# Kernel tuning notes

Hardware: AMD Instinct MI355X
Metric: run time of the kernel (lower is better)

Reference implementation:

```python
import jax, jax.numpy as jnp
import numpy as np

N = 10000      # nodes
E = 160000     # edges
IN = 256       # input feature dim
HID = 128      # hidden per head
H = 4          # heads (all layers)
EMB = 128      # dim_embedding (last-layer out per head)
SLOPE = 0.2    # leaky_relu negative slope in attention


def _gat_layer(h, src, dst, W, al, ar, b, residual, apply_act):
    """DGL-style GATConv (no dropout). h: [N, F_in], W: [F_in, H*D], al/ar/b: [H, D]."""
    n = h.shape[0]
    heads, d = al.shape
    feat = (h @ W).reshape(n, heads, d)                 # [N, H, D]
    el = jnp.sum(feat * al, axis=-1)                    # [N, H]
    er = jnp.sum(feat * ar, axis=-1)                    # [N, H]
    e = jax.nn.leaky_relu(el[src] + er[dst], SLOPE)     # [E, H]
    # edge softmax over incoming edges of dst (numerically stable)
    m = jax.ops.segment_max(e, dst, num_segments=n)
    m = jnp.where(jnp.isfinite(m), m, 0.0)              # empty segments -> 0
    ex = jnp.exp(e - m[dst])
    den = jax.ops.segment_sum(ex, dst, num_segments=n)
    alpha = ex / jnp.maximum(den[dst], 1e-9)            # [E, H]
    rst = jax.ops.segment_sum(alpha[:, :, None] * feat[src], dst, num_segments=n)  # [N, H, D]
    if residual:
        rst = rst + h.reshape(n, heads, d)              # identity residual (dims match)
    rst = rst + b
    return jax.nn.elu(rst) if apply_act else rst


def setup_inputs() -> dict:
    key = jax.random.key(0)
    ks = jax.random.split(key, 24)
    def p(k, shape, scale):
        return (jax.random.normal(k, shape, jnp.float32) * scale)
    inp = {
        'x': jax.random.normal(ks[0], (N, IN), jnp.float32),
        'src': jax.random.randint(ks[1], (E,), 0, N, dtype=jnp.int32).astype(jnp.int64),
        'dst': jax.random.randint(ks[2], (E,), 0, N, dtype=jnp.int32).astype(jnp.int64),
        # layer 0: in=IN, out=HID per head
        'W0': p(ks[3], (IN, H * HID), 1.0 / np.sqrt(IN)),
        'al0': p(ks[4], (H, HID), 0.1), 'ar0': p(ks[5], (H, HID), 0.1),
        'b0': p(ks[6], (H, HID), 0.02),
        # layer 1: in=H*HID=512, out=HID per head, residual
        'W1': p(ks[7], (H * HID, H * HID), 1.0 / np.sqrt(H * HID)),
        'al1': p(ks[8], (H, HID), 0.1), 'ar1': p(ks[9], (H, HID), 0.1),
        'b1': p(ks[10], (H, HID), 0.02),
        # layer 2: in=H*HID=512, out=EMB per head, residual, no activation
        'W2': p(ks[11], (H * HID, H * EMB), 1.0 / np.sqrt(H * HID)),
        'al2': p(ks[12], (H, EMB), 0.1), 'ar2': p(ks[13], (H, EMB), 0.1),
        'b2': p(ks[14], (H, EMB), 0.02),
        # MLP predictor: 2*EMB -> EMB -> EMB//2 -> 1
        'Wm0': p(ks[15], (2 * EMB, EMB), 1.0 / np.sqrt(2 * EMB)), 'bm0': p(ks[16], (EMB,), 0.02),
        'Wm1': p(ks[17], (EMB, EMB // 2), 1.0 / np.sqrt(EMB)), 'bm1': p(ks[18], (EMB // 2,), 0.02),
        'Wm2': p(ks[19], (EMB // 2, 1), 1.0 / np.sqrt(EMB // 2)), 'bm2': p(ks[20], (1,), 0.02),
    }
    return inp


def reference(x, src, dst, W0, al0, ar0, b0, W1, al1, ar1, b1, W2, al2, ar2, b2,
              Wm0, bm0, Wm1, bm1, Wm2, bm2):
    # GAT encoder
    h = _gat_layer(x, src, dst, W0, al0, ar0, b0, residual=False, apply_act=True).reshape(N, -1)
    h = _gat_layer(h, src, dst, W1, al1, ar1, b1, residual=True, apply_act=True).reshape(N, -1)
    h = _gat_layer(h, src, dst, W2, al2, ar2, b2, residual=True, apply_act=False).mean(axis=1)  # [N, EMB]
    # link predictor over all graph edges
    emb = jnp.concatenate([h[src], h[dst]], axis=1)     # [E, 2*EMB]
    z = jax.nn.relu(emb @ Wm0 + bm0)
    z = jax.nn.relu(z @ Wm1 + bm1)
    return jax.nn.sigmoid(z @ Wm2 + bm2)                # [E, 1]
```

## Files before the change

kernel.cpp:

```cpp
#include <hip/hip_runtime.h>
#include <hip/hip_bf16.h>
#include <math.h>

constexpr int kN = 10000;
constexpr int kE = 160000;
constexpr float kSlope = 0.2f;

typedef short v8s __attribute__((ext_vector_type(8)));
typedef float f32x4 __attribute__((ext_vector_type(4)));
typedef unsigned short ushort_t;

__device__ __forceinline__ float lrelu(float x) { return x > 0.f ? x : kSlope * x; }
__device__ __forceinline__ float elu_f(float x) { return x > 0.f ? x : (expf(x) - 1.f); }
__device__ __forceinline__ float b2f(ushort_t u) {
    return __uint_as_float(((unsigned)u) << 16);
}
__device__ __forceinline__ ushort_t f2b(float f) {
    unsigned u = __float_as_uint(f);
    return (ushort_t)((u + 0x7FFFu + ((u >> 16) & 1u)) >> 16);
}

__global__ void detect_flags(const void* __restrict__ x, const void* __restrict__ dsti,
                             int* __restrict__ flags) {
    __shared__ int sb[2];
    int tid = threadIdx.x;
    if (tid == 0) { sb[0] = 0; sb[1] = 0; }
    __syncthreads();
    const ushort_t* xb = (const ushort_t*)x;
    int big = 0;
    for (int i = tid; i < 4096; i += 256) {
        float v = b2f(xb[i]);
        if (!(fabsf(v) <= 1e4f)) big = 1;
    }
    const int* d32 = (const int*)dsti;
    int hi = 0;
    for (int i = tid; i < 4096; i += 256) hi |= d32[2 * i + 1];
    if (big) atomicOr(&sb[0], 1);
    if (hi)  atomicOr(&sb[1], 1);
    __syncthreads();
    if (tid == 0) { flags[0] = sb[0]; flags[1] = sb[1] ? 0 : 1; }
}

__global__ void zero_ints(int* __restrict__ p, int n) {
    int i = blockIdx.x * 256 + threadIdx.x;
    if (i < n) p[i] = 0;
}

__global__ void norm_idx2(const void* __restrict__ sin, const void* __restrict__ din,
                          int* __restrict__ nsrc, int* __restrict__ ndst,
                          const int* __restrict__ flags) {
    int i = blockIdx.x * 256 + threadIdx.x;
    if (i >= 2 * kE) return;
    const void* in = (i < kE) ? sin : din;
    int j = (i < kE) ? i : i - kE;
    int v = flags[1] ? (int)((const long long*)in)[j] : ((const int*)in)[j];
    v = ((unsigned)v < (unsigned)kN) ? v : 0;
    if (i < kE) nsrc[j] = v; else ndst[j] = v;
}

struct P13 { const void* p[13]; };
__global__ void cvt_small(P13 sp, float* __restrict__ dst, const int* __restrict__ flags) {
    int i = blockIdx.x * 256 + threadIdx.x;
    if (i >= 4865) return;
    int seg, offi;
    if (i < 4608)      { seg = i >> 9; offi = i & 511; }
    else if (i < 4736) { seg = 9;  offi = i - 4608; }
    else if (i < 4800) { seg = 10; offi = i - 4736; }
    else if (i < 4864) { seg = 11; offi = i - 4800; }
    else               { seg = 12; offi = 0; }
    dst[i] = flags[0] ? ((const float*)sp.p[seg])[offi]
                      : b2f(((const ushort_t*)sp.p[seg])[offi]);
}

__global__ void xprep(const void* __restrict__ in, ushort_t* __restrict__ out, int n,
                      const int* __restrict__ flags) {
    int i = blockIdx.x * 256 + threadIdx.x;
    if (i >= n) return;
    out[i] = flags[0] ? f2b(((const float*)in)[i]) : ((const ushort_t*)in)[i];
}

__global__ void wtprep(const void* __restrict__ W, ushort_t* __restrict__ WT,
                       int N, int Ksrc, int Kout, const int* __restrict__ flags) {
    int idx = blockIdx.x * 256 + threadIdx.x;
    if (idx >= N * Kout) return;
    int n = idx / Kout, k = idx - n * Kout;
    int srcidx = (k % Ksrc) * N + n;
    ushort_t v = flags[0] ? f2b(((const float*)W)[srcidx])
                          : ((const ushort_t*)W)[srcidx];
    WT[(size_t)n * Kout + k] = v;
}

__global__ void pqt_prep(const void* __restrict__ Wm0, ushort_t* __restrict__ PQT,
                         const int* __restrict__ flags) {
    int idx = blockIdx.x * 256 + threadIdx.x;
    if (idx >= 256 * 128) return;
    int n = idx >> 7, k = idx & 127;
    int srcidx = (k + ((n < 128) ? 0 : 128)) * 128 + (n & 127);
    ushort_t v = flags[0] ? f2b(((const float*)Wm0)[srcidx])
                          : ((const ushort_t*)Wm0)[srcidx];
    PQT[idx] = v;
}

__global__ void count_deg(const int* __restrict__ dst, int* __restrict__ deg, int n) {
    int i = blockIdx.x * 256 + threadIdx.x;
    if (i < n) atomicAdd(&deg[dst[i]], 1);
}

__global__ __launch_bounds__(1024) void scan_off(const int* __restrict__ deg,
                                                 int* __restrict__ off, int n) {
    __shared__ int s[1024];
    int tid = threadIdx.x;
    int per = (n + 1023) >> 10;
    int base = tid * per;
    int sum = 0;
    for (int i = 0; i < per; ++i) { int j = base + i; if (j < n) sum += deg[j]; }
    s[tid] = sum;
    __syncthreads();
    for (int d = 1; d < 1024; d <<= 1) {
        int v = (tid >= d) ? s[tid - d] : 0;
        __syncthreads();
        s[tid] += v;
        __syncthreads();
    }
    int run = (tid > 0) ? s[tid - 1] : 0;
    for (int i = 0; i < per; ++i) {
        int j = base + i;
        if (j < n) { off[j] = run; run += deg[j]; }
    }
    if (tid == 0) off[n] = s[1023];
}

__global__ void fill_csr(const int* __restrict__ src, const int* __restrict__ dst,
                         const int* __restrict__ off, int* __restrict__ cnt,
                         int* __restrict__ ss, int* __restrict__ eid,
                         int* __restrict__ dpos, int n) {
    int i = blockIdx.x * 256 + threadIdx.x;
    if (i < n) {
        int d = dst[i];
        int pos = off[d] + atomicAdd(&cnt[d], 1);
        if (pos < kE) { ss[pos] = src[i]; eid[pos] = i; dpos[pos] = d; }
    }
}

__global__ __launch_bounds__(256) void gemm_mfma(const ushort_t* __restrict__ A,
                                                 const ushort_t* __restrict__ WT,
                                                 void* __restrict__ Cout,
                                                 int M, int N, int K, int bf16out) {
    __shared__ __align__(16) ushort_t As[4][64][8];
    __shared__ __align__(16) ushort_t Bs[4][128][8];
    const int t = threadIdx.x;
    const int wave = t >> 6, lane = t & 63;
    const int l16 = lane & 15, q = lane >> 4;
    const int row0 = blockIdx.y * 64, col0 = blockIdx.x * 128;
    const int wm = (wave & 1) * 32, wn = (wave >> 1) * 64;
    const int am = t >> 2, ak8 = t & 3;
    const int sw = ak8 * 4;

    const ushort_t* aptr = A + (size_t)min(row0 + am, M - 1) * K + ak8 * 8;
    const ushort_t* bptr0 = WT + (size_t)(col0 + am) * K + ak8 * 8;
    const ushort_t* bptr1 = bptr0 + (size_t)64 * K;

    uint4 ga  = *(const uint4*)aptr;
    uint4 gb0 = *(const uint4*)bptr0;
    uint4 gb1 = *(const uint4*)bptr1;

    f32x4 acc[2][4];
#pragma unroll
    for (int mt = 0; mt < 2; ++mt)
#pragma unroll
        for (int nt = 0; nt < 4; ++nt)
#pragma unroll
            for (int r = 0; r < 4; ++r) acc[mt][nt][r] = 0.f;

    for (int k0 = 0; k0 < K; k0 += 32) {
        __syncthreads();
        *(uint4*)&As[ak8][am ^ sw][0] = ga;
        *(uint4*)&Bs[ak8][am ^ sw][0] = gb0;
        *(uint4*)&Bs[ak8][(am + 64) ^ sw][0] = gb1;
        __syncthreads();
        if (k0 + 32 < K) {
            ga  = *(const uint4*)(aptr + k0 + 32);
            gb0 = *(const uint4*)(bptr0 + k0 + 32);
            gb1 = *(const uint4*)(bptr1 + k0 + 32);
        }
        v8s af[2], bf[4];
        const int qs = q * 4;
#pragma unroll
        for (int mt = 0; mt < 2; ++mt)
            af[mt] = *(const v8s*)&As[q][(wm + mt * 16 + l16) ^ qs][0];
#pragma unroll
        for (int nt = 0; nt < 4; ++nt)
            bf[nt] = *(const v8s*)&Bs[q][(wn + nt * 16 + l16) ^ qs][0];
#pragma unroll
        for (int mt = 0; mt < 2; ++mt)
#pragma unroll
            for (int nt = 0; nt < 4; ++nt)
                acc[mt][nt] = __builtin_amdgcn_mfma_f32_16x16x32_bf16(af[mt], bf[nt],
                                                                      acc[mt][nt], 0, 0, 0);
    }
#pragma unroll
    for (int mt = 0; mt < 2; ++mt)
#pragma unroll
        for (int r = 0; r < 4; ++r) {
            int row = row0 + wm + mt * 16 + q * 4 + r;
            if (row < M) {
                if (bf16out) {
                    ushort_t* C = (ushort_t*)Cout;
#pragma unroll
                    for (int nt = 0; nt < 4; ++nt)
                        C[(size_t)row * N + col0 + wn + nt * 16 + l16] = f2b(acc[mt][nt][r]);
                } else {
                    float* C = (float*)Cout;
#pragma unroll
                    for (int nt = 0; nt < 4; ++nt)
                        C[(size_t)row * N + col0 + wn + nt * 16 + l16] = acc[mt][nt][r];
                }
            }
        }
}

__global__ __launch_bounds__(256) void compute_eler(const ushort_t* __restrict__ feat,
                                                    const float* __restrict__ al,
                                                    const float* __restrict__ ar,
                                                    float* __restrict__ el,
                                                    float* __restrict__ er) {
    int n = blockIdx.x;
    int h = threadIdx.x >> 6;
    int lane = threadIdx.x & 63;
    const ushort_t* f = feat + (size_t)n * 512 + h * 128;
    const float* a = al + h * 128;
    const float* r = ar + h * 128;
    ushort2 fv = *(const ushort2*)(f + 2 * lane);
    float f0 = b2f(fv.x), f1 = b2f(fv.y);
    float a0 = a[2 * lane], a1 = a[2 * lane + 1];
    float r0 = r[2 * lane], r1 = r[2 * lane + 1];
    float accl = f0 * a0 + f1 * a1;
    float accr = f0 * r0 + f1 * r1;
    for (int o = 32; o > 0; o >>= 1) {
        accl += __shfl_down(accl, o);
        accr += __shfl_down(accr, o);
    }
    if (lane == 0) { el[n * 4 + h] = accl; er[n * 4 + h] = accr; }
}

template <bool RES, bool ACT, int EPI>
__global__ __launch_bounds__(256) void gat_agg(const ushort_t* __restrict__ feat,
                                               const float* __restrict__ el,
                                               const float* __restrict__ er,
                                               const int* __restrict__ off,
                                               const int* __restrict__ ss,
                                               const float* __restrict__ resid,
                                               const float* __restrict__ bias,
                                               float* __restrict__ out,
                                               ushort_t* __restrict__ hl) {
    const int node = blockIdx.x * 4 + (threadIdx.x >> 6);
    const int lane = threadIdx.x & 63;
    if (node >= kN) return;
    const int off0 = off[node];
    const int deg = off[node + 1] - off0;
    float4 er4 = *(const float4*)(er + node * 4);

    float s0 = 0.f, s1 = 0.f, s2 = 0.f, s3 = 0.f;
    for (int i = lane; i < deg; i += 64) {
        int s = ss[off0 + i];
        float4 ev = *(const float4*)(el + s * 4);
        s0 += expf(lrelu(ev.x + er4.x));
        s1 += expf(lrelu(ev.y + er4.y));
        s2 += expf(lrelu(ev.z + er4.z));
        s3 += expf(lrelu(ev.w + er4.w));
    }
    for (int o = 1; o < 64; o <<= 1) {
        s0 += __shfl_xor(s0, o);
        s1 += __shfl_xor(s1, o);
        s2 += __shfl_xor(s2, o);
        s3 += __shfl_xor(s3, o);
    }
    const int head = lane >> 4;
    const float dh  = fmaxf((head == 0) ? s0 : (head == 1) ? s1 : (head == 2) ? s2 : s3, 1e-9f);
    const float erh = (head == 0) ? er4.x : (head == 1) ? er4.y : (head == 2) ? er4.z : er4.w;

    const int c0 = lane * 8;
    float acc[8] = {};
    for (int j = 0; j < deg; ++j) {
        int s = ss[off0 + j];
        float e = el[s * 4 + head];
        float wgt = expf(lrelu(e + erh)) / dh;
        const ushort_t* fp = feat + (size_t)s * 512 + c0;
        ushort4 u0 = *(const ushort4*)fp;
        ushort4 u1 = *(const ushort4*)(fp + 4);
        acc[0] += wgt * b2f(u0.x); acc[1] += wgt * b2f(u0.y);
        acc[2] += wgt * b2f(u0.z); acc[3] += wgt * b2f(u0.w);
        acc[4] += wgt * b2f(u1.x); acc[5] += wgt * b2f(u1.y);
        acc[6] += wgt * b2f(u1.z); acc[7] += wgt * b2f(u1.w);
    }
    float4 b0 = *(const float4*)(bias + c0);
    float4 b1 = *(const float4*)(bias + c0 + 4);
    float v[8] = {acc[0] + b0.x, acc[1] + b0.y, acc[2] + b0.z, acc[3] + b0.w,
                  acc[4] + b1.x, acc[5] + b1.y, acc[6] + b1.z, acc[7] + b1.w};
    if (RES) {
        const float* rp = resid + (size_t)node * 512 + c0;
        float4 r0 = *(const float4*)rp;
        float4 r1 = *(const float4*)(rp + 4);
        v[0] += r0.x; v[1] += r0.y; v[2] += r0.z; v[3] += r0.w;
        v[4] += r1.x; v[5] += r1.y; v[6] += r1.z; v[7] += r1.w;
    }
    if (ACT) {
#pragma unroll
        for (int r = 0; r < 8; ++r) v[r] = elu_f(v[r]);
    }
    if (EPI != 2) {
        float* op = out + (size_t)node * 512 + c0;
        *(float4*)op       = make_float4(v[0], v[1], v[2], v[3]);
        *(float4*)(op + 4) = make_float4(v[4], v[5], v[6], v[7]);
    }
    if (EPI == 1) {
        ushort_t* hp = hl + (size_t)node * 512 + c0;
        ushort4 h0 = {f2b(v[0]), f2b(v[1]), f2b(v[2]), f2b(v[3])};
        ushort4 h1 = {f2b(v[4]), f2b(v[5]), f2b(v[6]), f2b(v[7])};
        *(ushort4*)hp = h0;
        *(ushort4*)(hp + 4) = h1;
    }
    if (EPI == 2) {
        float m[8];
#pragma unroll
        for (int r = 0; r < 8; ++r) {
            float x = v[r] + __shfl_xor(v[r], 16);
            x += __shfl_xor(x, 32);
            m[r] = 0.25f * x;
        }
        if (lane < 16) {
            ushort_t* hp = hl + (size_t)node * 128 + lane * 8;
            ushort4 h0 = {f2b(m[0]), f2b(m[1]), f2b(m[2]), f2b(m[3])};
            ushort4 h1 = {f2b(m[4]), f2b(m[5]), f2b(m[6]), f2b(m[7])};
            *(ushort4*)hp = h0;
            *(ushort4*)(hp + 4) = h1;
        }
    }
}

__global__ __launch_bounds__(256) void edge_mfma(const ushort_t* __restrict__ PQb,
                                                 const float* __restrict__ bm0f,
                                                 const ushort_t* __restrict__ Wm1T,
                                                 const float* __restrict__ bm1f,
                                                 const float* __restrict__ wm2f,
                                                 const float* __restrict__ bm2f,
                                                 const int* __restrict__ ss,
                                                 const int* __restrict__ dpos,
                                                 const int* __restrict__ eid,
                                                 void* __restrict__ outv,
                                                 const int* __restrict__ flags) {
    __shared__ __align__(16) ushort_t zs[64][136];
    const int t = threadIdx.x;
    const int p0 = blockIdx.x * 64;
    const int c4 = (t & 31) * 4;
    float4 bb = *(const float4*)(bm0f + c4);
#pragma unroll
    for (int rep = 0; rep < 8; ++rep) {
        int e_l = rep * 8 + (t >> 5);
        int pos = p0 + e_l;
        int s = ss[pos], d = dpos[pos];
        ushort4 pv = *(const ushort4*)(PQb + (size_t)s * 256 + c4);
        ushort4 qv = *(const ushort4*)(PQb + (size_t)d * 256 + 128 + c4);
        ushort4 hi;
        hi.x = f2b(fmaxf(b2f(pv.x) + b2f(qv.x) + bb.x, 0.f));
        hi.y = f2b(fmaxf(b2f(pv.y) + b2f(qv.y) + bb.y, 0.f));
        hi.z = f2b(fmaxf(b2f(pv.z) + b2f(qv.z) + bb.z, 0.f));
        hi.w = f2b(fmaxf(b2f(pv.w) + b2f(qv.w) + bb.w, 0.f));
        *(ushort4*)&zs[e_l][c4] = hi;
    }
    __syncthreads();

    const int wave = t >> 6, lane = t & 63;
    const int l16 = lane & 15, q = lane >> 4;
    const int ew0 = wave * 16;
    f32x4 acc[4];
#pragma unroll
    for (int nt = 0; nt < 4; ++nt)
#pragma unroll
        for (int r = 0; r < 4; ++r) acc[nt][r] = 0.f;

#pragma unroll
    for (int ks = 0; ks < 4; ++ks) {
        int kq = ks * 32 + q * 8;
        v8s a = *(const v8s*)&zs[ew0 + l16][kq];
#pragma unroll
        for (int nt = 0; nt < 4; ++nt) {
            v8s b = *(const v8s*)(Wm1T + (size_t)(nt * 16 + l16) * 128 + kq);
            acc[nt] = __builtin_amdgcn_mfma_f32_16x16x32_bf16(a, b, acc[nt], 0, 0, 0);
        }
    }
    float b1v[4], w2v[4];
#pragma unroll
    for (int nt = 0; nt < 4; ++nt) {
        b1v[nt] = bm1f[nt * 16 + l16];
        w2v[nt] = wm2f[nt * 16 + l16];
    }
    float b2 = bm2f[0];
    const int f32out = flags[0];
#pragma unroll
    for (int r = 0; r < 4; ++r) {
        float v = 0.f;
#pragma unroll
        for (int nt = 0; nt < 4; ++nt)
            v += fmaxf(acc[nt][r] + b1v[nt], 0.f) * w2v[nt];
        v += __shfl_xor(v, 1);
        v += __shfl_xor(v, 2);
        v += __shfl_xor(v, 4);
        v += __shfl_xor(v, 8);
        if (l16 == 0) {
            int e = eid[p0 + ew0 + q * 4 + r];
            float rr = 1.f / (1.f + expf(-(v + b2)));
            if (f32out) ((float*)outv)[e] = rr;
            else        ((ushort_t*)outv)[e] = f2b(rr);
        }
    }
}

extern "C" void kernel_launch(void* const* d_in, const int* in_sizes, int n_in,
                              void* d_out, int out_size, void* d_ws, size_t ws_size,
                              hipStream_t stream) {
    (void)in_sizes; (void)n_in; (void)out_size; (void)ws_size;

    float* w = (float*)d_ws;
    size_t o = 0;
    auto alloc = [&](size_t n) { float* p = w + o; o += (n + 3) & ~size_t(3); return p; };
    float* smallb = alloc(4868);
    float* al0f = smallb + 0;    float* ar0f = smallb + 512;  float* b0f  = smallb + 1024;
    float* al1f = smallb + 1536; float* ar1f = smallb + 2048; float* b1f  = smallb + 2560;
    float* al2f = smallb + 3072; float* ar2f = smallb + 3584; float* b2f_ = smallb + 4096;
    float* bm0f = smallb + 4608; float* bm1f = smallb + 4736;
    float* wm2f = smallb + 4800; float* bm2f = smallb + 4864;
    float* elb  = alloc((size_t)kN * 4);
    float* erb  = alloc((size_t)kN * 4);
    ushort_t* Fb  = (ushort_t*)alloc((size_t)kN * 256);
    ushort_t* AHL = (ushort_t*)alloc((size_t)kN * 256);
    ushort_t* MHb = (ushort_t*)alloc((size_t)kN * 64);
    float* H0 = alloc((size_t)kN * 512);
    float* H1 = alloc((size_t)kN * 512);
    ushort_t* W0T  = (ushort_t*)alloc(65536);
    ushort_t* W1T  = (ushort_t*)alloc(131072);
    ushort_t* W2T  = (ushort_t*)alloc(131072);
    ushort_t* PQT  = (ushort_t*)alloc(16384);
    ushort_t* Wm1T = (ushort_t*)alloc(8192);
    int* ip    = (int*)(w + o);
    int* flags = ip;
    int* deg   = ip + 4;
    int* cnt   = deg + kN;
    int* off   = cnt + kN;
    int* ss    = off + 10004;
    int* eid   = ss + kE;
    int* dpos  = eid + kE;
    int* nsrc  = dpos + kE;
    int* ndst  = nsrc + kE;

    ushort_t* Xb  = (ushort_t*)H1;
    ushort_t* PQb = Fb;

    dim3 blk(256);

    detect_flags<<<dim3(1), blk, 0, stream>>>(d_in[0], d_in[2], flags);
    norm_idx2<<<dim3((2 * kE + 255) / 256), blk, 0, stream>>>(d_in[1], d_in[2], nsrc, ndst, flags);
    P13 sp;
    const int sidx[13] = {4, 5, 6, 8, 9, 10, 12, 13, 14, 16, 18, 19, 20};
    for (int i = 0; i < 13; ++i) sp.p[i] = d_in[sidx[i]];
    cvt_small<<<dim3(20), blk, 0, stream>>>(sp, smallb, flags);
    wtprep<<<dim3((512 * 256 + 255) / 256), blk, 0, stream>>>(d_in[3], W0T, 512, 256, 256, flags);
    wtprep<<<dim3((512 * 512 + 255) / 256), blk, 0, stream>>>(d_in[7], W1T, 512, 512, 512, flags);
    wtprep<<<dim3((512 * 512 + 255) / 256), blk, 0, stream>>>(d_in[11], W2T, 512, 512, 512, flags);
    pqt_prep<<<dim3(128), blk, 0, stream>>>(d_in[15], PQT, flags);
    wtprep<<<dim3((64 * 128 + 255) / 256), blk, 0, stream>>>(d_in[17], Wm1T, 64, 128, 128, flags);
    xprep<<<dim3((kN * 256 + 255) / 256), blk, 0, stream>>>(d_in[0], Xb, kN * 256, flags);

    zero_ints<<<dim3((2 * kN + 255) / 256), blk, 0, stream>>>(deg, 2 * kN);
    count_deg<<<dim3((kE + 255) / 256), blk, 0, stream>>>(ndst, deg, kE);
    scan_off<<<dim3(1), dim3(1024), 0, stream>>>(deg, off, kN);
    fill_csr<<<dim3((kE + 255) / 256), blk, 0, stream>>>(nsrc, ndst, off, cnt, ss, eid, dpos, kE);

    const int gy = (kN + 63) / 64;
    const int ga = (kN + 3) / 4;

    gemm_mfma<<<dim3(4, gy), blk, 0, stream>>>(Xb, W0T, Fb, kN, 512, 256, 1);
    compute_eler<<<dim3(kN), blk, 0, stream>>>(Fb, al0f, ar0f, elb, erb);
    gat_agg<false, true, 1><<<dim3(ga), blk, 0, stream>>>(Fb, elb, erb, off, ss,
                                                          nullptr, b0f, H0, AHL);

    gemm_mfma<<<dim3(4, gy), blk, 0, stream>>>(AHL, W1T, Fb, kN, 512, 512, 1);
    compute_eler<<<dim3(kN), blk, 0, stream>>>(Fb, al1f, ar1f, elb, erb);
    gat_agg<true, true, 1><<<dim3(ga), blk, 0, stream>>>(Fb, elb, erb, off, ss,
                                                         H0, b1f, H1, AHL);

    gemm_mfma<<<dim3(4, gy), blk, 0, stream>>>(AHL, W2T, Fb, kN, 512, 512, 1);
    compute_eler<<<dim3(kN), blk, 0, stream>>>(Fb, al2f, ar2f, elb, erb);
    gat_agg<true, false, 2><<<dim3(ga), blk, 0, stream>>>(Fb, elb, erb, off, ss,
                                                          H1, b2f_, nullptr, MHb);

    gemm_mfma<<<dim3(2, gy), blk, 0, stream>>>(MHb, PQT, PQb, kN, 256, 128, 1);

    edge_mfma<<<dim3(kE / 64), blk, 0, stream>>>(PQb, bm0f, Wm1T, bm1f, wm2f, bm2f,
                                                 ss, dpos, eid, d_out, flags);
}
```

Before: 381.9 us.

## Fuse prep kernels, single-pass edge softmax, bf16 residual in place

Merges flag detection with degree zeroing, and folds all weight, input and index conversion kernels plus degree counting into one prep launch, cutting launch count. The GAT aggregation now accumulates the softmax denominator in the same pass as the weighted feature sum, dropping the separate denominator loop, and prefetches the next source index. The residual is read from the bf16 activation buffer in place instead of separate fp32 H0/H1 buffers, so the fp32 output writes go away. The trade-off is lower residual precision. Normalisation also happens without max subtraction, as before.

```diff
diff --git a/kernel.cpp b/kernel.cpp
--- a/kernel.cpp
+++ b/kernel.cpp
@@ -20,90 +20,106 @@
     return (ushort_t)((u + 0x7FFFu + ((u >> 16) & 1u)) >> 16);
 }
 
-__global__ void detect_flags(const void* __restrict__ x, const void* __restrict__ dsti,
-                             int* __restrict__ flags) {
-    __shared__ int sb[2];
-    int tid = threadIdx.x;
-    if (tid == 0) { sb[0] = 0; sb[1] = 0; }
-    __syncthreads();
-    const ushort_t* xb = (const ushort_t*)x;
-    int big = 0;
-    for (int i = tid; i < 4096; i += 256) {
-        float v = b2f(xb[i]);
-        if (!(fabsf(v) <= 1e4f)) big = 1;
-    }
-    const int* d32 = (const int*)dsti;
-    int hi = 0;
-    for (int i = tid; i < 4096; i += 256) hi |= d32[2 * i + 1];
-    if (big) atomicOr(&sb[0], 1);
-    if (hi)  atomicOr(&sb[1], 1);
-    __syncthreads();
-    if (tid == 0) { flags[0] = sb[0]; flags[1] = sb[1] ? 0 : 1; }
-}
-
-__global__ void zero_ints(int* __restrict__ p, int n) {
+__global__ void detect_zero(const void* __restrict__ x, const void* __restrict__ dsti,
+                            int* __restrict__ flags, int* __restrict__ deg) {
+    if (blockIdx.x == 0) {
+        __shared__ int sb[2];
+        int tid = threadIdx.x;
+        if (tid == 0) { sb[0] = 0; sb[1] = 0; }
+        __syncthreads();
+        const ushort_t* xb = (const ushort_t*)x;
+        int big = 0;
+        for (int i = tid; i < 4096; i += 256) {
+            float v = b2f(xb[i]);
+            if (!(fabsf(v) <= 1e4f)) big = 1;
+        }
+        const int* d32 = (const int*)dsti;
+        int hi = 0;
+        for (int i = tid; i < 4096; i += 256) hi |= d32[2 * i + 1];
+        if (big) atomicOr(&sb[0], 1);
+        if (hi)  atomicOr(&sb[1], 1);
+        __syncthreads();
+        if (tid == 0) { flags[0] = sb[0]; flags[1] = sb[1] ? 0 : 1; }
+    } else {
+        int i = (blockIdx.x - 1) * 256 + threadIdx.x;
+        if (i < 2 * kN) deg[i] = 0;
+    }
+}
+
+struct PrepArgs {
+    const void* sm[13];
+    const void* W0; const void* W1; const void* W2; const void* Wm0; const void* Wm1;
+    const void* X; const void* srcIn; const void* dstIn;
+    float* smallb;
+    ushort_t* W0T; ushort_t* W1T; ushort_t* W2T; ushort_t* PQT; ushort_t* Wm1T;
+    ushort_t* Xb;
+    int* nsrc; int* ndst; int* deg;
+    const int* flags;
+};
+constexpr int kPrepTotal = 4865 + 131072 + 262144 + 262144 + 32768 + 8192 + 2560000 + 320000;
+
+__global__ void prep_all(PrepArgs a) {
     int i = blockIdx.x * 256 + threadIdx.x;
-    if (i < n) p[i] = 0;
-}
-
-__global__ void norm_idx2(const void* __restrict__ sin, const void* __restrict__ din,
-                          int* __restrict__ nsrc, int* __restrict__ ndst,
-                          const int* __restrict__ flags) {
-    int i = blockIdx.x * 256 + threadIdx.x;
-    if (i >= 2 * kE) return;
-    const void* in = (i < kE) ? sin : din;
-    int j = (i < kE) ? i : i - kE;
-    int v = flags[1] ? (int)((const long long*)in)[j] : ((const int*)in)[j];
-    v = ((unsigned)v < (unsigned)kN) ? v : 0;
-    if (i < kE) nsrc[j] = v; else ndst[j] = v;
-}
-
-struct P13 { const void* p[13]; };
-__global__ void cvt_small(P13 sp, float* __restrict__ dst, const int* __restrict__ flags) {
-    int i = blockIdx.x * 256 + threadIdx.x;
-    if (i >= 4865) return;
-    int seg, offi;
-    if (i < 4608)      { seg = i >> 9; offi = i & 511; }
-    else if (i < 4736) { seg = 9;  offi = i - 4608; }
-    else if (i < 4800) { seg = 10; offi = i - 4736; }
-    else if (i < 4864) { seg = 11; offi = i - 4800; }
-    else               { seg = 12; offi = 0; }
-    dst[i] = flags[0] ? ((const float*)sp.p[seg])[offi]
-                      : b2f(((const ushort_t*)sp.p[seg])[offi]);
-}
-
-__global__ void xprep(const void* __restrict__ in, ushort_t* __restrict__ out, int n,
-                      const int* __restrict__ flags) {
-    int i = blockIdx.x * 256 + threadIdx.x;
-    if (i >= n) return;
-    out[i] = flags[0] ? f2b(((const float*)in)[i]) : ((const ushort_t*)in)[i];
-}
-
-__global__ void wtprep(const void* __restrict__ W, ushort_t* __restrict__ WT,
-                       int N, int Ksrc, int Kout, const int* __restrict__ flags) {
-    int idx = blockIdx.x * 256 + threadIdx.x;
-    if (idx >= N * Kout) return;
-    int n = idx / Kout, k = idx - n * Kout;
-    int srcidx = (k % Ksrc) * N + n;
-    ushort_t v = flags[0] ? f2b(((const float*)W)[srcidx])
-                          : ((const ushort_t*)W)[srcidx];
-    WT[(size_t)n * Kout + k] = v;
-}
-
-__global__ void pqt_prep(const void* __restrict__ Wm0, ushort_t* __restrict__ PQT,
-                         const int* __restrict__ flags) {
-    int idx = blockIdx.x * 256 + threadIdx.x;
-    if (idx >= 256 * 128) return;
-    int n = idx >> 7, k = idx & 127;
-    int srcidx = (k + ((n < 128) ? 0 : 128)) * 128 + (n & 127);
-    ushort_t v = flags[0] ? f2b(((const float*)Wm0)[srcidx])
-                          : ((const ushort_t*)Wm0)[srcidx];
-    PQT[idx] = v;
-}
-
-__global__ void count_deg(const int* __restrict__ dst, int* __restrict__ deg, int n) {
-    int i = blockIdx.x * 256 + threadIdx.x;
-    if (i < n) atomicAdd(&deg[dst[i]], 1);
+    if (i >= kPrepTotal) return;
+    const int f32in = a.flags[0];
+    auto cv = [&](const void* p, int idx) -> ushort_t {
+        return f32in ? f2b(((const float*)p)[idx]) : ((const ushort_t*)p)[idx];
+    };
+    if (i < 4865) {
+        int seg, offi;
+        if (i < 4608)      { seg = i >> 9; offi = i & 511; }
+        else if (i < 4736) { seg = 9;  offi = i - 4608; }
+        else if (i < 4800) { seg = 10; offi = i - 4736; }
+        else if (i < 4864) { seg = 11; offi = i - 4800; }
+        else               { seg = 12; offi = 0; }
+        a.smallb[i] = f32in ? ((const float*)a.sm[seg])[offi]
+                            : b2f(((const ushort_t*)a.sm[seg])[offi]);
+        return;
+    }
+    i -= 4865;
+    if (i < 131072) {
+        int n = i >> 8, k = i & 255;
+        a.W0T[i] = cv(a.W0, k * 512 + n);
+        return;
+    }
+    i -= 131072;
+    if (i < 262144) {
+        int n = i >> 9, k = i & 511;
+        a.W1T[i] = cv(a.W1, k * 512 + n);
+        return;
+    }
+    i -= 262144;
+    if (i < 262144) {
+        int n = i >> 9, k = i & 511;
+        a.W2T[i] = cv(a.W2, k * 512 + n);
+        return;
+    }
+    i -= 262144;
+    if (i < 32768) {
+        int n = i >> 7, k = i & 127;
+        a.PQT[i] = cv(a.Wm0, (k + ((n < 128) ? 0 : 128)) * 128 + (n & 127));
+        return;
+    }
+    i -= 32768;
+    if (i < 8192) {
+        int n = i >> 7, k = i & 127;
+        a.Wm1T[i] = cv(a.Wm1, k * 64 + n);
+        return;
+    }
+    i -= 8192;
+    if (i < 2560000) {
+        a.Xb[i] = cv(a.X, i);
+        return;
+    }
+    i -= 2560000;
+    {
+        const void* in = (i < kE) ? a.srcIn : a.dstIn;
+        int j = (i < kE) ? i : i - kE;
+        int v = a.flags[1] ? (int)((const long long*)in)[j] : ((const int*)in)[j];
+        v = ((unsigned)v < (unsigned)kN) ? v : 0;
+        if (i < kE) a.nsrc[j] = v;
+        else { a.ndst[j] = v; atomicAdd(&a.deg[v], 1); }
+    }
 }
 
 __global__ __launch_bounds__(1024) void scan_off(const int* __restrict__ deg,
@@ -232,10 +248,8 @@
     const float* r = ar + h * 128;
     ushort2 fv = *(const ushort2*)(f + 2 * lane);
     float f0 = b2f(fv.x), f1 = b2f(fv.y);
-    float a0 = a[2 * lane], a1 = a[2 * lane + 1];
-    float r0 = r[2 * lane], r1 = r[2 * lane + 1];
-    float accl = f0 * a0 + f1 * a1;
-    float accr = f0 * r0 + f1 * r1;
+    float accl = f0 * a[2 * lane] + f1 * a[2 * lane + 1];
+    float accr = f0 * r[2 * lane] + f1 * r[2 * lane + 1];
     for (int o = 32; o > 0; o >>= 1) {
         accl += __shfl_down(accl, o);
         accr += __shfl_down(accr, o);
@@ -249,69 +263,53 @@
                                                const float* __restrict__ er,
                                                const int* __restrict__ off,
                                                const int* __restrict__ ss,
-                                               const float* __restrict__ resid,
+                                               const ushort_t* residb,
                                                const float* __restrict__ bias,
-                                               float* __restrict__ out,
-                                               ushort_t* __restrict__ hl) {
+                                               ushort_t* hl) {
     const int node = blockIdx.x * 4 + (threadIdx.x >> 6);
     const int lane = threadIdx.x & 63;
     if (node >= kN) return;
     const int off0 = off[node];
     const int deg = off[node + 1] - off0;
     float4 er4 = *(const float4*)(er + node * 4);
-
-    float s0 = 0.f, s1 = 0.f, s2 = 0.f, s3 = 0.f;
-    for (int i = lane; i < deg; i += 64) {
-        int s = ss[off0 + i];
-        float4 ev = *(const float4*)(el + s * 4);
-        s0 += expf(lrelu(ev.x + er4.x));
-        s1 += expf(lrelu(ev.y + er4.y));
-        s2 += expf(lrelu(ev.z + er4.z));
-        s3 += expf(lrelu(ev.w + er4.w));
-    }
-    for (int o = 1; o < 64; o <<= 1) {
-        s0 += __shfl_xor(s0, o);
-        s1 += __shfl_xor(s1, o);
-        s2 += __shfl_xor(s2, o);
-        s3 += __shfl_xor(s3, o);
-    }
     const int head = lane >> 4;
-    const float dh  = fmaxf((head == 0) ? s0 : (head == 1) ? s1 : (head == 2) ? s2 : s3, 1e-9f);
     const float erh = (head == 0) ? er4.x : (head == 1) ? er4.y : (head == 2) ? er4.z : er4.w;
 
     const int c0 = lane * 8;
+    float den = 0.f;
     float acc[8] = {};
+    int s_cur = (deg > 0) ? ss[off0] : 0;
     for (int j = 0; j < deg; ++j) {
-        int s = ss[off0 + j];
-        float e = el[s * 4 + head];
-        float wgt = expf(lrelu(e + erh)) / dh;
-        const ushort_t* fp = feat + (size_t)s * 512 + c0;
+        int s_nxt = (j + 1 < deg) ? ss[off0 + j + 1] : 0;
+        float e = el[s_cur * 4 + head];
+        float wgt = expf(lrelu(e + erh));
+        den += wgt;
+        const ushort_t* fp = feat + (size_t)s_cur * 512 + c0;
         ushort4 u0 = *(const ushort4*)fp;
         ushort4 u1 = *(const ushort4*)(fp + 4);
         acc[0] += wgt * b2f(u0.x); acc[1] += wgt * b2f(u0.y);
         acc[2] += wgt * b2f(u0.z); acc[3] += wgt * b2f(u0.w);
         acc[4] += wgt * b2f(u1.x); acc[5] += wgt * b2f(u1.y);
         acc[6] += wgt * b2f(u1.z); acc[7] += wgt * b2f(u1.w);
-    }
+        s_cur = s_nxt;
+    }
+    const float inv = 1.f / fmaxf(den, 1e-9f);
     float4 b0 = *(const float4*)(bias + c0);
     float4 b1 = *(const float4*)(bias + c0 + 4);
-    float v[8] = {acc[0] + b0.x, acc[1] + b0.y, acc[2] + b0.z, acc[3] + b0.w,
-                  acc[4] + b1.x, acc[5] + b1.y, acc[6] + b1.z, acc[7] + b1.w};
+    float v[8] = {acc[0] * inv + b0.x, acc[1] * inv + b0.y,
+                  acc[2] * inv + b0.z, acc[3] * inv + b0.w,
+                  acc[4] * inv + b1.x, acc[5] * inv + b1.y,
+                  acc[6] * inv + b1.z, acc[7] * inv + b1.w};
     if (RES) {
-        const float* rp = resid + (size_t)node * 512 + c0;
-        float4 r0 = *(const float4*)rp;
-        float4 r1 = *(const float4*)(rp + 4);
-        v[0] += r0.x; v[1] += r0.y; v[2] += r0.z; v[3] += r0.w;
-        v[4] += r1.x; v[5] += r1.y; v[6] += r1.z; v[7] += r1.w;
+        const ushort_t* rp = residb + (size_t)node * 512 + c0;
+        ushort4 r0 = *(const ushort4*)rp;
+        ushort4 r1 = *(const ushort4*)(rp + 4);
+        v[0] += b2f(r0.x); v[1] += b2f(r0.y); v[2] += b2f(r0.z); v[3] += b2f(r0.w);
+        v[4] += b2f(r1.x); v[5] += b2f(r1.y); v[6] += b2f(r1.z); v[7] += b2f(r1.w);
     }
     if (ACT) {
 #pragma unroll
         for (int r = 0; r < 8; ++r) v[r] = elu_f(v[r]);
-    }
-    if (EPI != 2) {
-        float* op = out + (size_t)node * 512 + c0;
-        *(float4*)op       = make_float4(v[0], v[1], v[2], v[3]);
-        *(float4*)(op + 4) = make_float4(v[4], v[5], v[6], v[7]);
     }
     if (EPI == 1) {
         ushort_t* hp = hl + (size_t)node * 512 + c0;
@@ -435,13 +433,12 @@
     ushort_t* Fb  = (ushort_t*)alloc((size_t)kN * 256);
     ushort_t* AHL = (ushort_t*)alloc((size_t)kN * 256);
     ushort_t* MHb = (ushort_t*)alloc((size_t)kN * 64);
-    float* H0 = alloc((size_t)kN * 512);
-    float* H1 = alloc((size_t)kN * 512);
+    ushort_t* Xb  = (ushort_t*)alloc((size_t)kN * 128);
     ushort_t* W0T  = (ushort_t*)alloc(65536);
     ushort_t* W1T  = (ushort_t*)alloc(131072);
     ushort_t* W2T  = (ushort_t*)alloc(131072);
     ushort_t* PQT  = (ushort_t*)alloc(16384);
-    ushort_t* Wm1T = (ushort_t*)alloc(8192);
+    ushort_t* Wm1T = (ushort_t*)alloc(4096);
     int* ip    = (int*)(w + o);
     int* flags = ip;
     int* deg   = ip + 4;
@@ -453,26 +450,21 @@
     int* nsrc  = dpos + kE;
     int* ndst  = nsrc + kE;
 
-    ushort_t* Xb  = (ushort_t*)H1;
     ushort_t* PQb = Fb;
 
     dim3 blk(256);
 
-    detect_flags<<<dim3(1), blk, 0, stream>>>(d_in[0], d_in[2], flags);
-    norm_idx2<<<dim3((2 * kE + 255) / 256), blk, 0, stream>>>(d_in[1], d_in[2], nsrc, ndst, flags);
-    P13 sp;
+    detect_zero<<<dim3(1 + (2 * kN + 255) / 256), blk, 0, stream>>>(d_in[0], d_in[2], flags, deg);
+
+    PrepArgs a;
     const int sidx[13] = {4, 5, 6, 8, 9, 10, 12, 13, 14, 16, 18, 19, 20};
-    for (int i = 0; i < 13; ++i) sp.p[i] = d_in[sidx[i]];
-    cvt_small<<<dim3(20), blk, 0, stream>>>(sp, smallb, flags);
-    wtprep<<<dim3((512 * 256 + 255) / 256), blk, 0, stream>>>(d_in[3], W0T, 512, 256, 256, flags);
-    wtprep<<<dim3((512 * 512 + 255) / 256), blk, 0, stream>>>(d_in[7], W1T, 512, 512, 512, flags);
-    wtprep<<<dim3((512 * 512 + 255) / 256), blk, 0, stream>>>(d_in[11], W2T, 512, 512, 512, flags);
-    pqt_prep<<<dim3(128), blk, 0, stream>>>(d_in[15], PQT, flags);
-    wtprep<<<dim3((64 * 128 + 255) / 256), blk, 0, stream>>>(d_in[17], Wm1T, 64, 128, 128, flags);
-    xprep<<<dim3((kN * 256 + 255) / 256), blk, 0, stream>>>(d_in[0], Xb, kN * 256, flags);
-
-    zero_ints<<<dim3((2 * kN + 255) / 256), blk, 0, stream>>>(deg, 2 * kN);
-    count_deg<<<dim3((kE + 255) / 256), blk, 0, stream>>>(ndst, deg, kE);
+    for (int i = 0; i < 13; ++i) a.sm[i] = d_in[sidx[i]];
+    a.W0 = d_in[3]; a.W1 = d_in[7]; a.W2 = d_in[11]; a.Wm0 = d_in[15]; a.Wm1 = d_in[17];
+    a.X = d_in[0]; a.srcIn = d_in[1]; a.dstIn = d_in[2];
+    a.smallb = smallb; a.W0T = W0T; a.W1T = W1T; a.W2T = W2T; a.PQT = PQT; a.Wm1T = Wm1T;
+    a.Xb = Xb; a.nsrc = nsrc; a.ndst = ndst; a.deg = deg; a.flags = flags;
+    prep_all<<<dim3((kPrepTotal + 255) / 256), blk, 0, stream>>>(a);
+
     scan_off<<<dim3(1), dim3(1024), 0, stream>>>(deg, off, kN);
     fill_csr<<<dim3((kE + 255) / 256), blk, 0, stream>>>(nsrc, ndst, off, cnt, ss, eid, dpos, kE);
 
@@ -482,17 +474,17 @@
     gemm_mfma<<<dim3(4, gy), blk, 0, stream>>>(Xb, W0T, Fb, kN, 512, 256, 1);
     compute_eler<<<dim3(kN), blk, 0, stream>>>(Fb, al0f, ar0f, elb, erb);
     gat_agg<false, true, 1><<<dim3(ga), blk, 0, stream>>>(Fb, elb, erb, off, ss,
-                                                          nullptr, b0f, H0, AHL);
+                                                          nullptr, b0f, AHL);
 
     gemm_mfma<<<dim3(4, gy), blk, 0, stream>>>(AHL, W1T, Fb, kN, 512, 512, 1);
     compute_eler<<<dim3(kN), blk, 0, stream>>>(Fb, al1f, ar1f, elb, erb);
     gat_agg<true, true, 1><<<dim3(ga), blk, 0, stream>>>(Fb, elb, erb, off, ss,
-                                                         H0, b1f, H1, AHL);
+                                                         AHL, b1f, AHL);
 
     gemm_mfma<<<dim3(4, gy), blk, 0, stream>>>(AHL, W2T, Fb, kN, 512, 512, 1);
     compute_eler<<<dim3(kN), blk, 0, stream>>>(Fb, al2f, ar2f, elb, erb);
     gat_agg<true, false, 2><<<dim3(ga), blk, 0, stream>>>(Fb, elb, erb, off, ss,
-                                                          H1, b2f_, nullptr, MHb);
+                                                          AHL, b2f_, MHb);
 
     gemm_mfma<<<dim3(2, gy), blk, 0, stream>>>(MHb, PQT, PQb, kN, 256, 128, 1);
 
```

Measured after the change: 360.5 us. 5.6% less time.
